# Kernel tuning notes

Measured on AMD Instinct MI355X. Metric: run time of the kernel, lower is better.

## Reference

```python
import jax, jax.numpy as jnp
import numpy as np

EMBED_DIM = 1024
NUM_HEADS = 16
D_K = EMBED_DIM // NUM_HEADS
SEQ = 4096
BATCH = 1


def setup_inputs() -> dict:
    key = jax.random.key(0)
    ks = jax.random.split(key, 9)
    s = 1.0 / np.sqrt(EMBED_DIM)
    return {
        "x": jax.random.normal(ks[0], (BATCH, SEQ, EMBED_DIM), dtype=jnp.float32),
        "Wq": jax.random.normal(ks[1], (EMBED_DIM, EMBED_DIM), dtype=jnp.float32) * s,
        "bq": jax.random.normal(ks[2], (EMBED_DIM,), dtype=jnp.float32) * 0.02,
        "Wk": jax.random.normal(ks[3], (EMBED_DIM, EMBED_DIM), dtype=jnp.float32) * s,
        "bk": jax.random.normal(ks[4], (EMBED_DIM,), dtype=jnp.float32) * 0.02,
        "Wv": jax.random.normal(ks[5], (EMBED_DIM, EMBED_DIM), dtype=jnp.float32) * s,
        "bv": jax.random.normal(ks[6], (EMBED_DIM,), dtype=jnp.float32) * 0.02,
        "Wo": jax.random.normal(ks[7], (EMBED_DIM, EMBED_DIM), dtype=jnp.float32) * s,
        "bo": jax.random.normal(ks[8], (EMBED_DIM,), dtype=jnp.float32) * 0.02,
    }


def reference(x, Wq, bq, Wk, bk, Wv, bv, Wo, bo):
    B, S, E = x.shape
    H, Dk = NUM_HEADS, D_K

    def split_heads(t):  # [B,S,E] -> [B,H,S,Dk]
        return t.reshape(B, S, H, Dk).transpose(0, 2, 1, 3)

    Q = split_heads(x @ Wq.T + bq)
    K = split_heads(x @ Wk.T + bk)
    V = split_heads(x @ Wv.T + bv)

    scores = jnp.einsum("bhqd,bhkd->bhqk", Q, K) / jnp.sqrt(jnp.float32(Dk))
    causal = jnp.tril(jnp.ones((S, S), dtype=bool))
    scores = jnp.where(causal, scores, -jnp.inf)
    attn = jax.nn.softmax(scores, axis=-1)
    out = jnp.einsum("bhqk,bhkd->bhqd", attn, V)  # [B,H,S,Dk]
    out = out.transpose(0, 2, 1, 3).reshape(B, S, E)
    return out @ Wo.T + bo
```

## Files before the change

kernel.cpp:

```cpp
#include <hip/hip_runtime.h>
#include <hip/hip_bf16.h>
#include <math.h>

#define SEQ 4096
#define EMB 1024
#define NH  16
#define DK  64

typedef __attribute__((ext_vector_type(8))) unsigned short us8;
typedef __attribute__((ext_vector_type(8))) short         s8;
typedef __attribute__((ext_vector_type(4))) unsigned short us4;
typedef __attribute__((ext_vector_type(4))) float          f4;

static __device__ __forceinline__ unsigned short f2bf(float f) {
    union { float f; unsigned u; } v; v.f = f;
    unsigned r = v.u + 0x7FFF + ((v.u >> 16) & 1);
    return (unsigned short)(r >> 16);
}

__device__ __forceinline__ void gl2lds16(const void* g, void* l) {
    __builtin_amdgcn_global_load_lds((const __attribute__((address_space(1))) void*)g,
                                     (__attribute__((address_space(3))) void*)l, 16, 0, 0);
}

__device__ __forceinline__ int pkbf(float a, float b) {
    return (int)__builtin_amdgcn_perm(__float_as_uint(a), __float_as_uint(b), 0x07060302u);
}

__global__ void cvt_all(const float* __restrict__ x,
                        const float* __restrict__ w0, const float* __restrict__ w1,
                        const float* __restrict__ w2, const float* __restrict__ w3,
                        unsigned short* __restrict__ xo,
                        unsigned short* __restrict__ o0, unsigned short* __restrict__ o1,
                        unsigned short* __restrict__ o2, unsigned short* __restrict__ o3) {
    const int idx = blockIdx.x * 256 + threadIdx.x;
    const float* in;
    unsigned short* out;
    int off;
    if (idx < (1 << 20)) { in = x; out = xo; off = idx; }
    else {
        const int t = idx - (1 << 20);
        const int w = t >> 18;
        off = t & ((1 << 18) - 1);
        in  = w == 0 ? w0 : (w == 1 ? w1 : (w == 2 ? w2 : w3));
        out = w == 0 ? o0 : (w == 1 ? o1 : (w == 2 ? o2 : o3));
    }
    const float4 v = ((const float4*)in)[off];
    us4 o;
    o[0] = f2bf(v.x); o[1] = f2bf(v.y); o[2] = f2bf(v.z); o[3] = f2bf(v.w);
    ((us4*)out)[off] = o;
}

__global__ __launch_bounds__(256) void transpose_kernel(
    const unsigned short* __restrict__ in, unsigned short* __restrict__ out) {
    __shared__ unsigned short t[64][72];
    const int tid = threadIdx.x;
    const int row = tid >> 2, c = (tid & 3) * 16;
    const int gr = blockIdx.x * 64, gc = blockIdx.y * 64;
    const unsigned short* src = in + (size_t)(gr + row) * EMB + gc + c;
    *(us8*)&t[row][c]     = *(const us8*)src;
    *(us8*)&t[row][c + 8] = *(const us8*)(src + 8);
    __syncthreads();
    us8 o0, o1;
#pragma unroll
    for (int j = 0; j < 8; ++j) { o0[j] = t[c + j][row]; o1[j] = t[c + 8 + j][row]; }
    const int a_   = c >> 4;
    const int base = (a_ >> 1) * 32 + (a_ & 1) * 4;
    us4 g0, g1, g2, g3;
#pragma unroll
    for (int i = 0; i < 4; ++i) { g0[i] = o0[i]; g1[i] = o0[4 + i]; g2[i] = o1[i]; g3[i] = o1[4 + i]; }
    unsigned short* dst = out + (size_t)(gc + row) * SEQ + gr + base;
    *(us4*)dst        = g0;
    *(us4*)(dst + 8)  = g1;
    *(us4*)(dst + 16) = g2;
    *(us4*)(dst + 24) = g3;
}

__global__ __launch_bounds__(256) void qkv_gemm(
    const unsigned short* __restrict__ X,
    const unsigned short* __restrict__ Wq, const unsigned short* __restrict__ Wk,
    const unsigned short* __restrict__ Wv,
    const float* __restrict__ bq, const float* __restrict__ bk, const float* __restrict__ bv,
    unsigned short* __restrict__ Qo, unsigned short* __restrict__ Ko, unsigned short* __restrict__ Vo)
{
    __shared__ unsigned short As[128 * 64];
    __shared__ unsigned short Bs[128 * 64];

    const int region = blockIdx.y >> 3;
    const unsigned short* W   = region == 0 ? Wq : (region == 1 ? Wk : Wv);
    const float*         bias = region == 0 ? bq : (region == 1 ? bk : bv);
    unsigned short*      out  = region == 0 ? Qo : (region == 1 ? Ko : Vo);
    const float scale = region == 0 ? 0.18033688011112042f : 1.0f;

    const int tid  = threadIdx.x;
    const int wave = tid >> 6;
    const int lane = tid & 63;
    const int quad = lane >> 4;
    const int l16  = lane & 15;
    const int wm   = (wave >> 1) * 64;
    const int wn   = (wave & 1) * 64;
    const int bm   = blockIdx.x * 128;
    const int bn   = (blockIdx.y & 7) * 128;

    f4 acc[4][4];
#pragma unroll
    for (int a = 0; a < 4; ++a)
#pragma unroll
        for (int b = 0; b < 4; ++b) acc[a][b] = (f4){0, 0, 0, 0};

    const int rsub = lane >> 3;
    const int gc   = ((lane & 7) ^ rsub) * 8;
    const int swz  = l16 & 7;

    for (int k0 = 0; k0 < EMB; k0 += 64) {
        __syncthreads();
#pragma unroll
        for (int i = 0; i < 4; ++i) {
            const int cb = i * 4 + wave;
            const int r  = cb * 8 + rsub;
            gl2lds16(X + (size_t)(bm + r) * EMB + k0 + gc, &As[cb * 512]);
            gl2lds16(W + (size_t)(bn + r) * EMB + k0 + gc, &Bs[cb * 512]);
        }
        __syncthreads();
#pragma unroll
        for (int kc = 0; kc < 2; ++kc) {
            s8 af[4], bf[4];
#pragma unroll
            for (int t = 0; t < 4; ++t) {
                const int seg = (kc * 4 + quad) ^ swz;
                af[t] = *(const s8*)&As[(wm + t * 16 + l16) * 64 + seg * 8];
                bf[t] = *(const s8*)&Bs[(wn + t * 16 + l16) * 64 + seg * 8];
            }
#pragma unroll
            for (int tm = 0; tm < 4; ++tm)
#pragma unroll
                for (int tn = 0; tn < 4; ++tn)
                    acc[tm][tn] = __builtin_amdgcn_mfma_f32_16x16x32_bf16(af[tm], bf[tn], acc[tm][tn], 0, 0, 0);
        }
    }

#pragma unroll
    for (int tn = 0; tn < 4; ++tn) {
        const int n = bn + wn + tn * 16 + l16;
        const float bv2 = bias[n];
#pragma unroll
        for (int tm = 0; tm < 4; ++tm)
#pragma unroll
            for (int rr = 0; rr < 4; ++rr) {
                const int m = bm + wm + tm * 16 + quad * 4 + rr;
                out[(size_t)m * EMB + n] = f2bf((acc[tm][tn][rr] + bv2) * scale);
            }
    }
}

__global__ __launch_bounds__(256) void gemm_op(
    const unsigned short* __restrict__ A, const unsigned short* __restrict__ B,
    const float* __restrict__ bias, float* __restrict__ C)
{
    __shared__ unsigned short As[128 * 64];
    __shared__ unsigned short Bs[64 * 64];

    const int tid  = threadIdx.x;
    const int wave = tid >> 6;
    const int lane = tid & 63;
    const int quad = lane >> 4;
    const int l16  = lane & 15;
    const int wm   = (wave >> 1) * 64;
    const int wn   = (wave & 1) * 32;
    const int bm   = blockIdx.x * 128;
    const int bn   = blockIdx.y * 64;

    f4 acc[4][2];
#pragma unroll
    for (int a = 0; a < 4; ++a) { acc[a][0] = (f4){0,0,0,0}; acc[a][1] = (f4){0,0,0,0}; }

    const int rsub = lane >> 3;
    const int gc   = ((lane & 7) ^ rsub) * 8;
    const int swz  = l16 & 7;

    for (int k0 = 0; k0 < EMB; k0 += 64) {
        __syncthreads();
#pragma unroll
        for (int i = 0; i < 6; ++i) {
            const int cb = i * 4 + wave;
            if (cb < 16) {
                gl2lds16(A + (size_t)(bm + cb * 8 + rsub) * EMB + k0 + gc, &As[cb * 512]);
            } else {
                const int c2 = cb - 16;
                gl2lds16(B + (size_t)(bn + c2 * 8 + rsub) * EMB + k0 + gc, &Bs[c2 * 512]);
            }
        }
        __syncthreads();
#pragma unroll
        for (int kc = 0; kc < 2; ++kc) {
            const int seg = (kc * 4 + quad) ^ swz;
            s8 af[4], bf[2];
#pragma unroll
            for (int t = 0; t < 4; ++t)
                af[t] = *(const s8*)&As[(wm + t * 16 + l16) * 64 + seg * 8];
#pragma unroll
            for (int t = 0; t < 2; ++t)
                bf[t] = *(const s8*)&Bs[(wn + t * 16 + l16) * 64 + seg * 8];
#pragma unroll
            for (int tm = 0; tm < 4; ++tm)
#pragma unroll
                for (int tn = 0; tn < 2; ++tn)
                    acc[tm][tn] = __builtin_amdgcn_mfma_f32_16x16x32_bf16(af[tm], bf[tn], acc[tm][tn], 0, 0, 0);
        }
    }

#pragma unroll
    for (int tn = 0; tn < 2; ++tn) {
        const int n = bn + wn + tn * 16 + l16;
        const float bv2 = bias[n];
#pragma unroll
        for (int tm = 0; tm < 4; ++tm)
#pragma unroll
            for (int rr = 0; rr < 4; ++rr) {
                const int m = bm + wm + tm * 16 + quad * 4 + rr;
                C[(size_t)m * EMB + n] = acc[tm][tn][rr] + bv2;
            }
    }
}

__global__ __launch_bounds__(256) void attn_kernel(
    const unsigned short* __restrict__ Qg, const unsigned short* __restrict__ Kg,
    const unsigned short* __restrict__ Vtg, unsigned short* __restrict__ Og)
{
    __shared__ unsigned short Ks[2][64][72];
    __shared__ unsigned short Vs[2][64][72];

    const int tid  = threadIdx.x;
    const int wave = tid >> 6;
    const int lane = tid & 63;
    const int quad = lane >> 4;
    const int l16  = lane & 15;
    const int h    = blockIdx.x;
    const int y    = blockIdx.y;
    const int u    = (y < 16) ? y : 47 - y;
    const int jmax = 63 - u;
    const int tileMine = (wave < 2) ? (63 - u) : u;
    const int jmine    = (wave < 2) ? jmax : u;
    const int colbase = h * DK;
    const int wrow0 = tileMine * 64 + (wave & 1) * 32;
    const int q_own = wrow0 + l16;

    s8 qf[2][2];
#pragma unroll
    for (int g2 = 0; g2 < 2; ++g2) {
        const unsigned short* q = Qg + (size_t)(q_own + 16 * g2) * EMB + colbase + quad * 8;
        qf[g2][0] = *(const s8*)(q);
        qf[g2][1] = *(const s8*)(q + 32);
    }

    const int row = tid >> 2;
    const int c0  = (tid & 3) * 16;
    const unsigned short* kptr = Kg  + (size_t)row * EMB + colbase + c0;
    const unsigned short* vptr = Vtg + (size_t)(colbase + row) * SEQ + c0;

    us8 kr0 = *(const us8*)kptr, kr1 = *(const us8*)(kptr + 8);
    us8 vr0 = *(const us8*)vptr, vr1 = *(const us8*)(vptr + 8);
    *(us8*)&Ks[0][row][c0]     = kr0;
    *(us8*)&Ks[0][row][c0 + 8] = kr1;
    *(us8*)&Vs[0][row][c0]     = vr0;
    *(us8*)&Vs[0][row][c0 + 8] = vr1;
    kr0 = *(const us8*)(kptr + (size_t)64 * EMB);
    kr1 = *(const us8*)(kptr + (size_t)64 * EMB + 8);
    vr0 = *(const us8*)(vptr + 64);
    vr1 = *(const us8*)(vptr + 64 + 8);

    float l_i[2] = {0.0f, 0.0f};
    f4 o[2][4];
#pragma unroll
    for (int g2 = 0; g2 < 2; ++g2)
#pragma unroll
        for (int t = 0; t < 4; ++t) o[g2][t] = (f4){0, 0, 0, 0};

    for (int j = 0; j <= jmax; ++j) {
        __syncthreads();
        const int cur = j & 1;
        if (j < jmax) {
            const int nxt = cur ^ 1;
            *(us8*)&Ks[nxt][row][c0]     = kr0;
            *(us8*)&Ks[nxt][row][c0 + 8] = kr1;
            *(us8*)&Vs[nxt][row][c0]     = vr0;
            *(us8*)&Vs[nxt][row][c0 + 8] = vr1;
            if (j + 1 < jmax) {
                const unsigned short* kn = kptr + (size_t)(j + 2) * 64 * EMB;
                const unsigned short* vn = vptr + (j + 2) * 64;
                kr0 = *(const us8*)kn;  kr1 = *(const us8*)(kn + 8);
                vr0 = *(const us8*)vn;  vr1 = *(const us8*)(vn + 8);
            }
        }

        if (j <= jmine) {
            f4 s[2][4];
#pragma unroll
            for (int g2 = 0; g2 < 2; ++g2)
#pragma unroll
                for (int t = 0; t < 4; ++t) s[g2][t] = (f4){0, 0, 0, 0};
#pragma unroll
            for (int kc = 0; kc < 2; ++kc)
#pragma unroll
                for (int t = 0; t < 4; ++t) {
                    s8 kv = *(const s8*)&Ks[cur][t * 16 + l16][kc * 32 + quad * 8];
                    s[0][t] = __builtin_amdgcn_mfma_f32_16x16x32_bf16(kv, qf[0][kc], s[0][t], 0, 0, 0);
                    s[1][t] = __builtin_amdgcn_mfma_f32_16x16x32_bf16(kv, qf[1][kc], s[1][t], 0, 0, 0);
                }

            if (j == jmine) {
#pragma unroll
                for (int t = 0; t < 4; ++t) {
                    const int kb = j * 64 + t * 16 + quad * 4;
#pragma unroll
                    for (int r = 0; r < 4; ++r) {
                        if (kb + r > q_own)      s[0][t][r] = -1e30f;
                        if (kb + r > q_own + 16) s[1][t][r] = -1e30f;
                    }
                }
            }

            union { int i[8]; s8 v[2]; } pku[2];
#pragma unroll
            for (int g2 = 0; g2 < 2; ++g2) {
                float rs = 0.0f;
#pragma unroll
                for (int t = 0; t < 4; ++t)
#pragma unroll
                    for (int r = 0; r < 4; ++r) {
                        const float p = __builtin_amdgcn_exp2f(s[g2][t][r]);
                        s[g2][t][r] = p;
                        rs += p;
                    }
                rs += __shfl_xor(rs, 16);
                rs += __shfl_xor(rs, 32);
                l_i[g2] += rs;
#pragma unroll
                for (int t = 0; t < 4; ++t) {
                    pku[g2].i[t * 2]     = pkbf(s[g2][t][1], s[g2][t][0]);
                    pku[g2].i[t * 2 + 1] = pkbf(s[g2][t][3], s[g2][t][2]);
                }
            }

#pragma unroll
            for (int kc = 0; kc < 2; ++kc)
#pragma unroll
                for (int t = 0; t < 4; ++t) {
                    s8 va = *(const s8*)&Vs[cur][t * 16 + l16][kc * 32 + quad * 8];
                    o[0][t] = __builtin_amdgcn_mfma_f32_16x16x32_bf16(va, pku[0].v[kc], o[0][t], 0, 0, 0);
                    o[1][t] = __builtin_amdgcn_mfma_f32_16x16x32_bf16(va, pku[1].v[kc], o[1][t], 0, 0, 0);
                }
        }
    }

#pragma unroll
    for (int g2 = 0; g2 < 2; ++g2) {
        const float inv = 1.0f / l_i[g2];
#pragma unroll
        for (int t = 0; t < 4; ++t) {
            us4 ov;
#pragma unroll
            for (int r = 0; r < 4; ++r) ov[r] = f2bf(o[g2][t][r] * inv);
            *(us4*)&Og[(size_t)(q_own + 16 * g2) * EMB + colbase + t * 16 + quad * 4] = ov;
        }
    }
}

extern "C" void kernel_launch(void* const* d_in, const int* in_sizes, int n_in,
                              void* d_out, int out_size, void* d_ws, size_t ws_size,
                              hipStream_t stream) {
    const float* x  = (const float*)d_in[0];
    const float* Wq = (const float*)d_in[1];
    const float* bq = (const float*)d_in[2];
    const float* Wk = (const float*)d_in[3];
    const float* bk = (const float*)d_in[4];
    const float* Wv = (const float*)d_in[5];
    const float* bv = (const float*)d_in[6];
    const float* Wo = (const float*)d_in[7];
    const float* bo = (const float*)d_in[8];
    float* out = (float*)d_out;

    unsigned short* ws = (unsigned short*)d_ws;
    unsigned short* xb  = ws;
    unsigned short* Wqb = xb  + (size_t)SEQ * EMB;
    unsigned short* Wkb = Wqb + (size_t)EMB * EMB;
    unsigned short* Wvb = Wkb + (size_t)EMB * EMB;
    unsigned short* Wob = Wvb + (size_t)EMB * EMB;
    unsigned short* Qb  = Wob + (size_t)EMB * EMB;
    unsigned short* Kb  = Qb  + (size_t)SEQ * EMB;
    unsigned short* Vtb = Kb  + (size_t)SEQ * EMB;
    unsigned short* Ab  = Vtb + (size_t)SEQ * EMB;

    cvt_all<<<8192, 256, 0, stream>>>(x, Wq, Wk, Wv, Wo, xb, Wqb, Wkb, Wvb, Wob);

    qkv_gemm<<<dim3(SEQ / 128, 24), 256, 0, stream>>>(xb, Wqb, Wkb, Wvb, bq, bk, bv, Qb, Kb, Ab);

    transpose_kernel<<<dim3(SEQ / 64, EMB / 64), 256, 0, stream>>>(Ab, Vtb);

    attn_kernel<<<dim3(NH, 32), 256, 0, stream>>>(Qb, Kb, Vtb, Ab);

    gemm_op<<<dim3(SEQ / 128, EMB / 64), 256, 0, stream>>>(Ab, Wob, bo, out);
}
```

Measured before the change: 227.3 us.

## Split attention KV tiles across wave pairs by parity and merge partials in LDS

Doubles the attention block to 512 threads. Each query-row group is now handled by two waves that take alternating (even/odd) KV tiles, so per-wave serial work is halved. The partial O accumulators and row sums are combined through a new LDS buffer after the loop. This appears to rely on the softmax not tracking a running max, so the partials can simply be added. The cost is extra LDS use (about 35KB more), fewer resident blocks per CU, and an extra reduction step with two block barriers.

Result: faster. 221.9 us (-2.4%).

```diff
diff --git a/kernel.cpp b/kernel.cpp
--- a/kernel.cpp
+++ b/kernel.cpp
@@ -223,12 +223,13 @@
     }
 }
 
-__global__ __launch_bounds__(256) void attn_kernel(
+__global__ __launch_bounds__(512) void attn_kernel(
     const unsigned short* __restrict__ Qg, const unsigned short* __restrict__ Kg,
     const unsigned short* __restrict__ Vtg, unsigned short* __restrict__ Og)
 {
     __shared__ unsigned short Ks[2][64][72];
     __shared__ unsigned short Vs[2][64][72];
+    __shared__ float Om[4][34][64];
 
     const int tid  = threadIdx.x;
     const int wave = tid >> 6;
@@ -239,10 +240,11 @@
     const int y    = blockIdx.y;
     const int u    = (y < 16) ? y : 47 - y;
     const int jmax = 63 - u;
-    const int tileMine = (wave < 2) ? (63 - u) : u;
-    const int jmine    = (wave < 2) ? jmax : u;
+    const int myTile = (wave < 4) ? (63 - u) : u;
+    const int parity = (wave >> 1) & 1;
+    const int half   = wave & 1;
     const int colbase = h * DK;
-    const int wrow0 = tileMine * 64 + (wave & 1) * 32;
+    const int wrow0 = myTile * 64 + half * 32;
     const int q_own = wrow0 + l16;
 
     s8 qf[2][2];
@@ -253,21 +255,17 @@
         qf[g2][1] = *(const s8*)(q + 32);
     }
 
-    const int row = tid >> 2;
-    const int c0  = (tid & 3) * 16;
+    const int row = tid >> 3;
+    const int c0  = (tid & 7) * 8;
     const unsigned short* kptr = Kg  + (size_t)row * EMB + colbase + c0;
     const unsigned short* vptr = Vtg + (size_t)(colbase + row) * SEQ + c0;
 
-    us8 kr0 = *(const us8*)kptr, kr1 = *(const us8*)(kptr + 8);
-    us8 vr0 = *(const us8*)vptr, vr1 = *(const us8*)(vptr + 8);
-    *(us8*)&Ks[0][row][c0]     = kr0;
-    *(us8*)&Ks[0][row][c0 + 8] = kr1;
-    *(us8*)&Vs[0][row][c0]     = vr0;
-    *(us8*)&Vs[0][row][c0 + 8] = vr1;
-    kr0 = *(const us8*)(kptr + (size_t)64 * EMB);
-    kr1 = *(const us8*)(kptr + (size_t)64 * EMB + 8);
-    vr0 = *(const us8*)(vptr + 64);
-    vr1 = *(const us8*)(vptr + 64 + 8);
+    us8 kr = *(const us8*)kptr;
+    us8 vr = *(const us8*)vptr;
+    *(us8*)&Ks[0][row][c0] = kr;
+    *(us8*)&Vs[0][row][c0] = vr;
+    kr = *(const us8*)(kptr + (size_t)64 * EMB);
+    vr = *(const us8*)(vptr + 64);
 
     float l_i[2] = {0.0f, 0.0f};
     f4 o[2][4];
@@ -281,19 +279,15 @@
         const int cur = j & 1;
         if (j < jmax) {
             const int nxt = cur ^ 1;
-            *(us8*)&Ks[nxt][row][c0]     = kr0;
-            *(us8*)&Ks[nxt][row][c0 + 8] = kr1;
-            *(us8*)&Vs[nxt][row][c0]     = vr0;
-            *(us8*)&Vs[nxt][row][c0 + 8] = vr1;
+            *(us8*)&Ks[nxt][row][c0] = kr;
+            *(us8*)&Vs[nxt][row][c0] = vr;
             if (j + 1 < jmax) {
-                const unsigned short* kn = kptr + (size_t)(j + 2) * 64 * EMB;
-                const unsigned short* vn = vptr + (j + 2) * 64;
-                kr0 = *(const us8*)kn;  kr1 = *(const us8*)(kn + 8);
-                vr0 = *(const us8*)vn;  vr1 = *(const us8*)(vn + 8);
-            }
-        }
-
-        if (j <= jmine) {
+                kr = *(const us8*)(kptr + (size_t)(j + 2) * 64 * EMB);
+                vr = *(const us8*)(vptr + (j + 2) * 64);
+            }
+        }
+
+        if ((j & 1) == parity && j <= myTile) {
             f4 s[2][4];
 #pragma unroll
             for (int g2 = 0; g2 < 2; ++g2)
@@ -308,7 +302,7 @@
                     s[1][t] = __builtin_amdgcn_mfma_f32_16x16x32_bf16(kv, qf[1][kc], s[1][t], 0, 0, 0);
                 }
 
-            if (j == jmine) {
+            if (j == myTile) {
 #pragma unroll
                 for (int t = 0; t < 4; ++t) {
                     const int kb = j * 64 + t * 16 + quad * 4;
@@ -353,15 +347,40 @@
         }
     }
 
-#pragma unroll
-    for (int g2 = 0; g2 < 2; ++g2) {
-        const float inv = 1.0f / l_i[g2];
-#pragma unroll
-        for (int t = 0; t < 4; ++t) {
-            us4 ov;
-#pragma unroll
-            for (int r = 0; r < 4; ++r) ov[r] = f2bf(o[g2][t][r] * inv);
-            *(us4*)&Og[(size_t)(q_own + 16 * g2) * EMB + colbase + t * 16 + quad * 4] = ov;
+    const int idx = ((wave >> 2) << 1) | half;
+    __syncthreads();
+    if (parity) {
+#pragma unroll
+        for (int g2 = 0; g2 < 2; ++g2) {
+#pragma unroll
+            for (int t = 0; t < 4; ++t)
+#pragma unroll
+                for (int r = 0; r < 4; ++r)
+                    Om[idx][g2 * 16 + t * 4 + r][lane] = o[g2][t][r];
+            Om[idx][32 + g2][lane] = l_i[g2];
+        }
+    }
+    __syncthreads();
+    if (!parity) {
+#pragma unroll
+        for (int g2 = 0; g2 < 2; ++g2) {
+#pragma unroll
+            for (int t = 0; t < 4; ++t)
+#pragma unroll
+                for (int r = 0; r < 4; ++r)
+                    o[g2][t][r] += Om[idx][g2 * 16 + t * 4 + r][lane];
+            l_i[g2] += Om[idx][32 + g2][lane];
+        }
+#pragma unroll
+        for (int g2 = 0; g2 < 2; ++g2) {
+            const float inv = 1.0f / l_i[g2];
+#pragma unroll
+            for (int t = 0; t < 4; ++t) {
+                us4 ov;
+#pragma unroll
+                for (int r = 0; r < 4; ++r) ov[r] = f2bf(o[g2][t][r] * inv);
+                *(us4*)&Og[(size_t)(q_own + 16 * g2) * EMB + colbase + t * 16 + quad * 4] = ov;
+            }
         }
     }
 }
@@ -397,7 +416,7 @@
 
     transpose_kernel<<<dim3(SEQ / 64, EMB / 64), 256, 0, stream>>>(Ab, Vtb);
 
-    attn_kernel<<<dim3(NH, 32), 256, 0, stream>>>(Qb, Kb, Vtb, Ab);
+    attn_kernel<<<dim3(NH, 32), 512, 0, stream>>>(Qb, Kb, Vtb, Ab);
 
     gemm_op<<<dim3(SEQ / 128, EMB / 64), 256, 0, stream>>>(Ab, Wob, bo, out);
 }
```
